# Kernel optimization log

Measured on AMD Instinct MI355X. Metric: run time of the kernel, lower is better.

## Reference

```python
import jax, jax.numpy as jnp
import numpy as np

N_NODES = 50000
N_EDGES = 800000
LEAKY_SLOPE = 0.2


def _gcn_conv(x, src, dst, W, b, n_nodes):
    """DGL GraphConv with norm='both': D_out^{-1/2} -> SpMM -> D_in^{-1/2} -> XW+b.
    Degrees clamped to min 1 as in DGL."""
    ones = jnp.ones(src.shape[0], dtype=x.dtype)
    out_deg = jnp.clip(jax.ops.segment_sum(ones, src, num_segments=n_nodes), 1.0)
    in_deg = jnp.clip(jax.ops.segment_sum(ones, dst, num_segments=n_nodes), 1.0)
    xs = x * jax.lax.rsqrt(out_deg)[:, None]          # [N, F] source-side norm
    agg = jax.ops.segment_sum(xs[src], dst, num_segments=n_nodes)  # SpMM: [N, F]
    agg = agg * jax.lax.rsqrt(in_deg)[:, None]        # dest-side norm
    return agg @ W + b


def setup_inputs() -> dict:
    key = jax.random.key(0)
    ks = jax.random.split(key, 13)
    d_in, d_hid, d_out = 300, 400, 512
    sc_in, sc_hid = 1.0 / np.sqrt(d_in), 1.0 / np.sqrt(d_hid)
    return {
        "init_emb": jax.random.normal(ks[0], (N_NODES, d_in), jnp.float32),
        "Wa1": jax.random.normal(ks[1], (d_in, d_hid), jnp.float32) * sc_in,
        "ba1": jnp.zeros((d_hid,), jnp.float32),
        "Wa2": jax.random.normal(ks[2], (d_hid, d_out), jnp.float32) * sc_hid,
        "ba2": jnp.zeros((d_out,), jnp.float32),
        "Wb1": jax.random.normal(ks[3], (d_in, d_hid), jnp.float32) * sc_in,
        "bb1": jnp.zeros((d_hid,), jnp.float32),
        "Wb2": jax.random.normal(ks[4], (d_hid, d_out), jnp.float32) * sc_hid,
        "bb2": jnp.zeros((d_out,), jnp.float32),
        "src1": jax.random.randint(ks[5], (N_EDGES,), 0, N_NODES, jnp.int32),
        "dst1": jax.random.randint(ks[6], (N_EDGES,), 0, N_NODES, jnp.int32),
        "src2": jax.random.randint(ks[7], (N_EDGES,), 0, N_NODES, jnp.int32),
        "dst2": jax.random.randint(ks[8], (N_EDGES,), 0, N_NODES, jnp.int32),
    }


def reference(init_emb, Wa1, ba1, Wa2, ba2, Wb1, bb1, Wb2, bb2,
              src1, dst1, src2, dst2):
    n = init_emb.shape[0]
    # hop 1 (dropout=0.0 -> identity)
    x1 = jax.nn.leaky_relu(_gcn_conv(init_emb, src1, dst1, Wa1, ba1, n), LEAKY_SLOPE)
    x2 = jax.nn.leaky_relu(_gcn_conv(init_emb, src2, dst2, Wb1, bb1, n), LEAKY_SLOPE)
    x = x1 + x2
    # hop 2
    y1 = _gcn_conv(x, src1, dst1, Wa2, ba2, n)
    y2 = _gcn_conv(x, src2, dst2, Wb2, bb2, n)
    return y1 + y2
```

## Files before the change

### kernel.cpp

```cpp
#include <hip/hip_runtime.h>

#define NN 50000
#define NE 800000
#define LEAKY 0.2f

using bf16x8 = __attribute__((ext_vector_type(8))) short;
using f32x4  = __attribute__((ext_vector_type(4))) float;

static __device__ __forceinline__ unsigned short f2bf(float f) {
  unsigned u = __float_as_uint(f);
  u += 0x7FFF + ((u >> 16) & 1);
  return (unsigned short)(u >> 16);
}
static __device__ __forceinline__ float bf2f(unsigned short h) {
  return __uint_as_float((unsigned)h << 16);
}

__global__ void zero_ints(int* __restrict__ p, int n) {
  int i = blockIdx.x * blockDim.x + threadIdx.x;
  int s = gridDim.x * blockDim.x;
  for (; i < n; i += s) p[i] = 0;
}

__global__ void deg_kernel(const int* __restrict__ s1, const int* __restrict__ d1,
                           const int* __restrict__ s2, const int* __restrict__ d2,
                           int* od1, int* id1, int* od2, int* id2) {
  int i = blockIdx.x * blockDim.x + threadIdx.x;
  int st = gridDim.x * blockDim.x;
  for (int e = i; e < NE; e += st) {
    int a = s1[e], b = d1[e], c = s2[e], d = d2[e];
    atomicAdd(&od1[a], 1);
    atomicAdd(&id1[b], 1);
    atomicAdd(&od2[c], 1);
    atomicAdd(&id2[d], 1);
  }
}

__global__ void scale_kernel(const int* __restrict__ od1, const int* __restrict__ id1,
                             const int* __restrict__ od2, const int* __restrict__ id2,
                             float* io1, float* ii1, float* io2, float* ii2) {
  int i = blockIdx.x * blockDim.x + threadIdx.x;
  if (i < NN) {
    io1[i] = rsqrtf((float)(od1[i] > 0 ? od1[i] : 1));
    ii1[i] = rsqrtf((float)(id1[i] > 0 ? id1[i] : 1));
    io2[i] = rsqrtf((float)(od2[i] > 0 ? od2[i] : 1));
    ii2[i] = rsqrtf((float)(id2[i] > 0 ? id2[i] : 1));
  }
}

__global__ void scan_kernel(const int* __restrict__ id1, const int* __restrict__ id2,
                            int* rp1, int* rp2) {
  const int* deg = blockIdx.x ? id2 : id1;
  int* rp = blockIdx.x ? rp2 : rp1;
  __shared__ int sm[1024];
  __shared__ int carry;
  int t = threadIdx.x;
  if (t == 0) carry = 0;
  __syncthreads();
  for (int base = 0; base < NN; base += 1024) {
    int v = (base + t < NN) ? deg[base + t] : 0;
    sm[t] = v;
    __syncthreads();
    #pragma unroll
    for (int o = 1; o < 1024; o <<= 1) {
      int add = (t >= o) ? sm[t - o] : 0;
      __syncthreads();
      sm[t] += add;
      __syncthreads();
    }
    if (base + t < NN) rp[base + t] = carry + sm[t] - v;
    __syncthreads();
    if (t == 0) carry += sm[1023];
    __syncthreads();
  }
  if (t == 0) rp[NN] = carry;
}

__global__ void fill_kernel(const int* __restrict__ s1, const int* __restrict__ d1,
                            const int* __restrict__ s2, const int* __restrict__ d2,
                            const int* __restrict__ rp1, const int* __restrict__ rp2,
                            int* fill1, int* fill2, int* col1, int* col2) {
  int i = blockIdx.x * blockDim.x + threadIdx.x;
  int st = gridDim.x * blockDim.x;
  for (int e = i; e < NE; e += st) {
    int sa = s1[e], da = d1[e], sb = s2[e], db = d2[e];
    int pa = atomicAdd(&fill1[da], 1);
    int pb = atomicAdd(&fill2[db], 1);
    col1[rp1[da] + pa] = sa;
    col2[rp2[db] + pb] = sb;
  }
}

template <int F>
__global__ __launch_bounds__(256) void spmm_kernel(
    const float* __restrict__ x, const int* __restrict__ rp, const int* __restrict__ col,
    const float* __restrict__ inv_out, const float* __restrict__ inv_in,
    float* __restrict__ outbuf) {
  constexpr int F4 = F / 4;
  constexpr int NI = (F4 + 63) / 64;
  int gw = (blockIdx.x * blockDim.x + threadIdx.x) >> 6;
  int lane = threadIdx.x & 63;
  int nw = (gridDim.x * blockDim.x) >> 6;
  const float4* __restrict__ x4 = (const float4*)x;
  float4* __restrict__ o4 = (float4*)outbuf;
  for (int node = gw; node < NN; node += nw) {
    float4 acc[NI];
    #pragma unroll
    for (int i = 0; i < NI; ++i) acc[i] = make_float4(0.f, 0.f, 0.f, 0.f);
    int beg = rp[node], end = rp[node + 1];
    for (int j = beg; j < end; ++j) {
      int s = col[j];
      float w = inv_out[s];
      #pragma unroll
      for (int i = 0; i < NI; ++i) {
        int idx = i * 64 + lane;
        if (idx < F4) {
          float4 v = x4[(size_t)s * F4 + idx];
          acc[i].x += v.x * w;
          acc[i].y += v.y * w;
          acc[i].z += v.z * w;
          acc[i].w += v.w * w;
        }
      }
    }
    float wi = inv_in[node];
    #pragma unroll
    for (int i = 0; i < NI; ++i) {
      int idx = i * 64 + lane;
      if (idx < F4) {
        float4 v = acc[i];
        v.x *= wi; v.y *= wi; v.z *= wi; v.w *= wi;
        o4[(size_t)node * F4 + idx] = v;
      }
    }
  }
}

__global__ void wsplit(const float* __restrict__ W, short* __restrict__ Wh,
                       short* __restrict__ Wl, int K, int Nc, int KB) {
  int total = 4 * KB * 4096;
  int i = blockIdx.x * blockDim.x + threadIdx.x;
  int st = gridDim.x * blockDim.x;
  for (; i < total; i += st) {
    int chunk = i >> 12;
    int e = i & 4095;
    int kk = e >> 7;
    int rn = e & 127;
    int nb = chunk / KB;
    int kb = chunk - nb * KB;
    int n = nb * 128 + rn;
    int k = kb * 32 + kk;
    float v = (n < Nc && k < K) ? W[(size_t)k * Nc + n] : 0.f;
    unsigned short h = f2bf(v);
    unsigned short l = f2bf(v - bf2f(h));
    size_t o = ((size_t)chunk * 128 + rn) * 32 + kk;
    Wh[o] = (short)h;
    Wl[o] = (short)l;
  }
}

template <int EPI, int DUAL>
__global__ __launch_bounds__(256, 2) void mgemm(
    const float* __restrict__ A1, const float* __restrict__ A2,
    const short* __restrict__ W1h, const short* __restrict__ W1l,
    const short* __restrict__ W2h, const short* __restrict__ W2l,
    const float* __restrict__ b1, const float* __restrict__ b2,
    const float* __restrict__ T, float* __restrict__ out,
    int M, int K, int Nc, int KB) {
  __shared__ short Ah[128 * 40];
  __shared__ short Al[128 * 40];
  __shared__ short Bh[128 * 40];
  __shared__ short Bl[128 * 40];

  const int tid = threadIdx.x;
  const int m0 = blockIdx.y * 128;
  const int nb = blockIdx.x;
  const int n0 = nb * 128;

  const int lane = tid & 63;
  const int wid = tid >> 6;
  const int wr = (wid >> 1) * 64;
  const int wc = (wid & 1) * 64;
  const int lr = lane & 15;
  const int lk = (lane >> 4) * 8;

  f32x4 acc[4][4];
  #pragma unroll
  for (int i = 0; i < 4; ++i)
    #pragma unroll
    for (int j = 0; j < 4; ++j) acc[i][j] = (f32x4)(0.f);

  const int sr = tid >> 1;
  const int sk = (tid & 1) * 16;

  for (int kb = 0; kb < KB; ++kb) {
    {
      const float* arow = A1 + (size_t)(m0 + sr) * K + kb * 32 + sk;
      bool rok = (m0 + sr) < M;
      #pragma unroll
      for (int i4 = 0; i4 < 4; ++i4) {
        int kg = kb * 32 + sk + i4 * 4;
        float4 v = make_float4(0.f, 0.f, 0.f, 0.f);
        if (rok && kg + 4 <= K) v = *(const float4*)(arow + i4 * 4);
        unsigned short hx = f2bf(v.x), hy = f2bf(v.y), hz = f2bf(v.z), hw = f2bf(v.w);
        short4 h = make_short4((short)hx, (short)hy, (short)hz, (short)hw);
        short4 l = make_short4((short)f2bf(v.x - bf2f(hx)), (short)f2bf(v.y - bf2f(hy)),
                               (short)f2bf(v.z - bf2f(hz)), (short)f2bf(v.w - bf2f(hw)));
        *(short4*)&Ah[sr * 40 + sk + i4 * 4] = h;
        *(short4*)&Al[sr * 40 + sk + i4 * 4] = l;
      }
      size_t wbase = (((size_t)nb * KB + kb) << 12) + sr * 32 + sk;
      const uint4* sh = (const uint4*)(W1h + wbase);
      const uint4* sl = (const uint4*)(W1l + wbase);
      *(uint4*)&Bh[sr * 40 + sk]     = sh[0];
      *(uint4*)&Bh[sr * 40 + sk + 8] = sh[1];
      *(uint4*)&Bl[sr * 40 + sk]     = sl[0];
      *(uint4*)&Bl[sr * 40 + sk + 8] = sl[1];
    }
    __syncthreads();
    {
      bf16x8 fah[4], fal[4], fbh[4], fbl[4];
      #pragma unroll
      for (int i = 0; i < 4; ++i) {
        fah[i] = *(const bf16x8*)&Ah[(wr + i * 16 + lr) * 40 + lk];
        fal[i] = *(const bf16x8*)&Al[(wr + i * 16 + lr) * 40 + lk];
      }
      #pragma unroll
      for (int j = 0; j < 4; ++j) {
        fbh[j] = *(const bf16x8*)&Bh[(wc + j * 16 + lr) * 40 + lk];
        fbl[j] = *(const bf16x8*)&Bl[(wc + j * 16 + lr) * 40 + lk];
      }
      #pragma unroll
      for (int i = 0; i < 4; ++i)
        #pragma unroll
        for (int j = 0; j < 4; ++j) {
          acc[i][j] = __builtin_amdgcn_mfma_f32_16x16x32_bf16(fah[i], fbh[j], acc[i][j], 0, 0, 0);
          acc[i][j] = __builtin_amdgcn_mfma_f32_16x16x32_bf16(fah[i], fbl[j], acc[i][j], 0, 0, 0);
          acc[i][j] = __builtin_amdgcn_mfma_f32_16x16x32_bf16(fal[i], fbh[j], acc[i][j], 0, 0, 0);
        }
    }
    __syncthreads();
    if (DUAL) {
      {
        const float* arow = A2 + (size_t)(m0 + sr) * K + kb * 32 + sk;
        bool rok = (m0 + sr) < M;
        #pragma unroll
        for (int i4 = 0; i4 < 4; ++i4) {
          int kg = kb * 32 + sk + i4 * 4;
          float4 v = make_float4(0.f, 0.f, 0.f, 0.f);
          if (rok && kg + 4 <= K) v = *(const float4*)(arow + i4 * 4);
          unsigned short hx = f2bf(v.x), hy = f2bf(v.y), hz = f2bf(v.z), hw = f2bf(v.w);
          short4 h = make_short4((short)hx, (short)hy, (short)hz, (short)hw);
          short4 l = make_short4((short)f2bf(v.x - bf2f(hx)), (short)f2bf(v.y - bf2f(hy)),
                                 (short)f2bf(v.z - bf2f(hz)), (short)f2bf(v.w - bf2f(hw)));
          *(short4*)&Ah[sr * 40 + sk + i4 * 4] = h;
          *(short4*)&Al[sr * 40 + sk + i4 * 4] = l;
        }
        size_t wbase = (((size_t)nb * KB + kb) << 12) + sr * 32 + sk;
        const uint4* sh = (const uint4*)(W2h + wbase);
        const uint4* sl = (const uint4*)(W2l + wbase);
        *(uint4*)&Bh[sr * 40 + sk]     = sh[0];
        *(uint4*)&Bh[sr * 40 + sk + 8] = sh[1];
        *(uint4*)&Bl[sr * 40 + sk]     = sl[0];
        *(uint4*)&Bl[sr * 40 + sk + 8] = sl[1];
      }
      __syncthreads();
      {
        bf16x8 fah[4], fal[4], fbh[4], fbl[4];
        #pragma unroll
        for (int i = 0; i < 4; ++i) {
          fah[i] = *(const bf16x8*)&Ah[(wr + i * 16 + lr) * 40 + lk];
          fal[i] = *(const bf16x8*)&Al[(wr + i * 16 + lr) * 40 + lk];
        }
        #pragma unroll
        for (int j = 0; j < 4; ++j) {
          fbh[j] = *(const bf16x8*)&Bh[(wc + j * 16 + lr) * 40 + lk];
          fbl[j] = *(const bf16x8*)&Bl[(wc + j * 16 + lr) * 40 + lk];
        }
        #pragma unroll
        for (int i = 0; i < 4; ++i)
          #pragma unroll
          for (int j = 0; j < 4; ++j) {
            acc[i][j] = __builtin_amdgcn_mfma_f32_16x16x32_bf16(fah[i], fbh[j], acc[i][j], 0, 0, 0);
            acc[i][j] = __builtin_amdgcn_mfma_f32_16x16x32_bf16(fah[i], fbl[j], acc[i][j], 0, 0, 0);
            acc[i][j] = __builtin_amdgcn_mfma_f32_16x16x32_bf16(fal[i], fbh[j], acc[i][j], 0, 0, 0);
          }
      }
      __syncthreads();
    }
  }

  #pragma unroll
  for (int i = 0; i < 4; ++i) {
    #pragma unroll
    for (int rr = 0; rr < 4; ++rr) {
      int r = m0 + wr + i * 16 + (lane >> 4) * 4 + rr;
      if (r >= M) continue;
      #pragma unroll
      for (int j = 0; j < 4; ++j) {
        int c = n0 + wc + j * 16 + lr;
        if (c >= Nc) continue;
        float v = acc[i][j][rr] + b1[c];
        if (DUAL) v += b2[c];
        if (EPI == 0 || EPI == 1) v = v > 0.f ? v : LEAKY * v;
        if (EPI == 1) v += T[(size_t)r * Nc + c];
        out[(size_t)r * Nc + c] = v;
      }
    }
  }
}

extern "C" void kernel_launch(void* const* d_in, const int* in_sizes, int n_in,
                              void* d_out, int out_size, void* d_ws, size_t ws_size,
                              hipStream_t stream) {
  const float* emb = (const float*)d_in[0];
  const float* Wa1 = (const float*)d_in[1];
  const float* ba1 = (const float*)d_in[2];
  const float* Wa2 = (const float*)d_in[3];
  const float* ba2 = (const float*)d_in[4];
  const float* Wb1 = (const float*)d_in[5];
  const float* bb1 = (const float*)d_in[6];
  const float* Wb2 = (const float*)d_in[7];
  const float* bb2 = (const float*)d_in[8];
  const int* src1 = (const int*)d_in[9];
  const int* dst1 = (const int*)d_in[10];
  const int* src2 = (const int*)d_in[11];
  const int* dst2 = (const int*)d_in[12];
  float* out = (float*)d_out;

  char* ws = (char*)d_ws;
  size_t off = 0;
  auto alloc = [&](size_t nbytes) -> void* {
    off = (off + 255) & ~(size_t)255;
    void* p = ws + off;
    off += nbytes;
    return p;
  };
  int* od1 = (int*)alloc(NN * 4);
  int* id1 = (int*)alloc(NN * 4);
  int* od2 = (int*)alloc(NN * 4);
  int* id2 = (int*)alloc(NN * 4);
  int* fill1 = (int*)alloc(NN * 4);
  int* fill2 = (int*)alloc(NN * 4);
  int* rp1 = (int*)alloc((NN + 1) * 4);
  int* rp2 = (int*)alloc((NN + 1) * 4);
  int* col1 = (int*)alloc((size_t)NE * 4);
  int* col2 = (int*)alloc((size_t)NE * 4);
  float* io1 = (float*)alloc(NN * 4);
  float* ii1 = (float*)alloc(NN * 4);
  float* io2 = (float*)alloc(NN * 4);
  float* ii2 = (float*)alloc(NN * 4);
  const int KB1 = 10;
  const int KB2 = 13;
  short* Wa1h = (short*)alloc((size_t)4 * KB1 * 4096 * 2);
  short* Wa1l = (short*)alloc((size_t)4 * KB1 * 4096 * 2);
  short* Wb1h = (short*)alloc((size_t)4 * KB1 * 4096 * 2);
  short* Wb1l = (short*)alloc((size_t)4 * KB1 * 4096 * 2);
  short* Wa2h = (short*)alloc((size_t)4 * KB2 * 4096 * 2);
  short* Wa2l = (short*)alloc((size_t)4 * KB2 * 4096 * 2);
  short* Wb2h = (short*)alloc((size_t)4 * KB2 * 4096 * 2);
  short* Wb2l = (short*)alloc((size_t)4 * KB2 * 4096 * 2);
  float* bufA1 = (float*)alloc((size_t)NN * 400 * 4);
  float* bufA2 = (float*)alloc((size_t)NN * 400 * 4);
  float* X = (float*)d_out;

  int nz = (int)(((char*)fill2 - (char*)od1) / 4) + NN;
  zero_ints<<<256, 256, 0, stream>>>(od1, nz);

  deg_kernel<<<1024, 256, 0, stream>>>(src1, dst1, src2, dst2, od1, id1, od2, id2);
  scale_kernel<<<(NN + 255) / 256, 256, 0, stream>>>(od1, id1, od2, id2, io1, ii1, io2, ii2);
  scan_kernel<<<2, 1024, 0, stream>>>(id1, id2, rp1, rp2);
  fill_kernel<<<1024, 256, 0, stream>>>(src1, dst1, src2, dst2, rp1, rp2,
                                        fill1, fill2, col1, col2);

  wsplit<<<640, 256, 0, stream>>>(Wa1, Wa1h, Wa1l, 300, 400, KB1);
  wsplit<<<640, 256, 0, stream>>>(Wb1, Wb1h, Wb1l, 300, 400, KB1);
  wsplit<<<832, 256, 0, stream>>>(Wa2, Wa2h, Wa2l, 400, 512, KB2);
  wsplit<<<832, 256, 0, stream>>>(Wb2, Wb2h, Wb2l, 400, 512, KB2);

  dim3 gg(4, (NN + 127) / 128);

  spmm_kernel<300><<<12500, 256, 0, stream>>>(emb, rp1, col1, io1, ii1, bufA1);
  mgemm<0, 0><<<gg, 256, 0, stream>>>(bufA1, nullptr, Wa1h, Wa1l, nullptr, nullptr,
                                      ba1, nullptr, nullptr, X, NN, 300, 400, KB1);
  spmm_kernel<300><<<12500, 256, 0, stream>>>(emb, rp2, col2, io2, ii2, bufA2);
  mgemm<1, 0><<<gg, 256, 0, stream>>>(bufA2, nullptr, Wb1h, Wb1l, nullptr, nullptr,
                                      bb1, nullptr, X, X, NN, 300, 400, KB1);

  spmm_kernel<400><<<12500, 256, 0, stream>>>(X, rp1, col1, io1, ii1, bufA1);
  spmm_kernel<400><<<12500, 256, 0, stream>>>(X, rp2, col2, io2, ii2, bufA2);
  mgemm<2, 1><<<gg, 256, 0, stream>>>(bufA1, bufA2, Wa2h, Wa2l, Wb2h, Wb2l,
                                      ba2, bb2, nullptr, out, NN, 400, 512, KB2);
}
```

Baseline: 1.734 ms.

## Emit bf16 hi/lo split from SpMM and widen GEMM tiles to 128x256

The SpMM epilogue now writes padded bf16 hi/lo pairs directly, so the GEMM no longer reads fp32 activations and converts them per tile. Weights are pre-arranged in an MFMA-fragment-friendly layout, and the GEMM uses 128x256 tiles with 8 accumulator columns per wave and an XCD-aware workgroup remap. The main intent is fewer global bytes read per GEMM and less conversion work. The cost is more registers and less occupancy (the launch-bounds min-blocks hint is removed) plus extra bytes written by the SpMM.

```diff
diff --git a/kernel.cpp b/kernel.cpp
--- a/kernel.cpp
+++ b/kernel.cpp
@@ -91,18 +91,18 @@
   }
 }
 
-template <int F>
+template <int F, int KP>
 __global__ __launch_bounds__(256) void spmm_kernel(
     const float* __restrict__ x, const int* __restrict__ rp, const int* __restrict__ col,
     const float* __restrict__ inv_out, const float* __restrict__ inv_in,
-    float* __restrict__ outbuf) {
+    short* __restrict__ hi, short* __restrict__ lo) {
   constexpr int F4 = F / 4;
-  constexpr int NI = (F4 + 63) / 64;
+  constexpr int P4 = KP / 4;
+  constexpr int NI = (P4 + 63) / 64;
   int gw = (blockIdx.x * blockDim.x + threadIdx.x) >> 6;
   int lane = threadIdx.x & 63;
   int nw = (gridDim.x * blockDim.x) >> 6;
   const float4* __restrict__ x4 = (const float4*)x;
-  float4* __restrict__ o4 = (float4*)outbuf;
   for (int node = gw; node < NN; node += nw) {
     float4 acc[NI];
     #pragma unroll
@@ -127,10 +127,15 @@
     #pragma unroll
     for (int i = 0; i < NI; ++i) {
       int idx = i * 64 + lane;
-      if (idx < F4) {
+      if (idx < P4) {
         float4 v = acc[i];
         v.x *= wi; v.y *= wi; v.z *= wi; v.w *= wi;
-        o4[(size_t)node * F4 + idx] = v;
+        unsigned short hx = f2bf(v.x), hy = f2bf(v.y), hz = f2bf(v.z), hw = f2bf(v.w);
+        short4 h = make_short4((short)hx, (short)hy, (short)hz, (short)hw);
+        short4 l = make_short4((short)f2bf(v.x - bf2f(hx)), (short)f2bf(v.y - bf2f(hy)),
+                               (short)f2bf(v.z - bf2f(hz)), (short)f2bf(v.w - bf2f(hw)));
+        *(short4*)&hi[(size_t)node * KP + idx * 4] = h;
+        *(short4*)&lo[(size_t)node * KP + idx * 4] = l;
       }
     }
   }
@@ -138,153 +143,111 @@
 
 __global__ void wsplit(const float* __restrict__ W, short* __restrict__ Wh,
                        short* __restrict__ Wl, int K, int Nc, int KB) {
-  int total = 4 * KB * 4096;
+  int total = 2 * KB * 8192;
   int i = blockIdx.x * blockDim.x + threadIdx.x;
   int st = gridDim.x * blockDim.x;
   for (; i < total; i += st) {
-    int chunk = i >> 12;
-    int e = i & 4095;
-    int kk = e >> 7;
-    int rn = e & 127;
-    int nb = chunk / KB;
-    int kb = chunk - nb * KB;
-    int n = nb * 128 + rn;
+    int c2 = i >> 13;
+    int e = i & 8191;
+    int kk = e >> 8;
+    int rn = e & 255;
+    int nb2 = c2 / KB;
+    int kb = c2 - nb2 * KB;
+    int n = nb2 * 256 + rn;
     int k = kb * 32 + kk;
     float v = (n < Nc && k < K) ? W[(size_t)k * Nc + n] : 0.f;
     unsigned short h = f2bf(v);
     unsigned short l = f2bf(v - bf2f(h));
-    size_t o = ((size_t)chunk * 128 + rn) * 32 + kk;
+    size_t o = (size_t)c2 * 8192 + (rn >> 4) * 512 + ((kk >> 3) * 16 + (rn & 15)) * 8 + (kk & 7);
     Wh[o] = (short)h;
     Wl[o] = (short)l;
   }
 }
 
 template <int EPI, int DUAL>
-__global__ __launch_bounds__(256, 2) void mgemm(
-    const float* __restrict__ A1, const float* __restrict__ A2,
+__global__ __launch_bounds__(256) void mgemm(
+    const short* __restrict__ A1h, const short* __restrict__ A1l,
+    const short* __restrict__ A2h, const short* __restrict__ A2l,
     const short* __restrict__ W1h, const short* __restrict__ W1l,
     const short* __restrict__ W2h, const short* __restrict__ W2l,
     const float* __restrict__ b1, const float* __restrict__ b2,
     const float* __restrict__ T, float* __restrict__ out,
-    int M, int K, int Nc, int KB) {
-  __shared__ short Ah[128 * 40];
-  __shared__ short Al[128 * 40];
-  __shared__ short Bh[128 * 40];
-  __shared__ short Bl[128 * 40];
+    int M, int Nc, int KB, int KP) {
+  __shared__ short Ah[4096], Al[4096];
+  __shared__ short Bh[8192], Bl[8192];
 
   const int tid = threadIdx.x;
-  const int m0 = blockIdx.y * 128;
-  const int nb = blockIdx.x;
-  const int n0 = nb * 128;
+  const int nwg = gridDim.x;
+  const int q = nwg >> 3, r = nwg & 7;
+  const int xcd = blockIdx.x & 7, loc = blockIdx.x >> 3;
+  const int wgid = ((xcd < r) ? xcd * (q + 1) : r * (q + 1) + (xcd - r) * q) + loc;
+  const int nb = wgid & 1;
+  const int m0 = (wgid >> 1) * 128;
+  const int n0 = nb * 256;
 
   const int lane = tid & 63;
   const int wid = tid >> 6;
   const int wr = (wid >> 1) * 64;
-  const int wc = (wid & 1) * 64;
-  const int lr = lane & 15;
-  const int lk = (lane >> 4) * 8;
-
-  f32x4 acc[4][4];
+  const int wc = (wid & 1) * 128;
+
+  f32x4 acc[4][8];
   #pragma unroll
   for (int i = 0; i < 4; ++i)
     #pragma unroll
-    for (int j = 0; j < 4; ++j) acc[i][j] = (f32x4)(0.f);
-
-  const int sr = tid >> 1;
-  const int sk = (tid & 1) * 16;
+    for (int j = 0; j < 8; ++j) acc[i][j] = (f32x4)(0.f);
 
   for (int kb = 0; kb < KB; ++kb) {
-    {
-      const float* arow = A1 + (size_t)(m0 + sr) * K + kb * 32 + sk;
-      bool rok = (m0 + sr) < M;
+    #pragma unroll
+    for (int ch = 0; ch < 1 + DUAL; ++ch) {
+      const short* __restrict__ Asrch = ch ? A2h : A1h;
+      const short* __restrict__ Asrcl = ch ? A2l : A1l;
+      const short* __restrict__ Wsrch = ch ? W2h : W1h;
+      const short* __restrict__ Wsrcl = ch ? W2l : W1l;
       #pragma unroll
-      for (int i4 = 0; i4 < 4; ++i4) {
-        int kg = kb * 32 + sk + i4 * 4;
-        float4 v = make_float4(0.f, 0.f, 0.f, 0.f);
-        if (rok && kg + 4 <= K) v = *(const float4*)(arow + i4 * 4);
-        unsigned short hx = f2bf(v.x), hy = f2bf(v.y), hz = f2bf(v.z), hw = f2bf(v.w);
-        short4 h = make_short4((short)hx, (short)hy, (short)hz, (short)hw);
-        short4 l = make_short4((short)f2bf(v.x - bf2f(hx)), (short)f2bf(v.y - bf2f(hy)),
-                               (short)f2bf(v.z - bf2f(hz)), (short)f2bf(v.w - bf2f(hw)));
-        *(short4*)&Ah[sr * 40 + sk + i4 * 4] = h;
-        *(short4*)&Al[sr * 40 + sk + i4 * 4] = l;
-      }
-      size_t wbase = (((size_t)nb * KB + kb) << 12) + sr * 32 + sk;
-      const uint4* sh = (const uint4*)(W1h + wbase);
-      const uint4* sl = (const uint4*)(W1l + wbase);
-      *(uint4*)&Bh[sr * 40 + sk]     = sh[0];
-      *(uint4*)&Bh[sr * 40 + sk + 8] = sh[1];
-      *(uint4*)&Bl[sr * 40 + sk]     = sl[0];
-      *(uint4*)&Bl[sr * 40 + sk + 8] = sl[1];
-    }
-    __syncthreads();
-    {
-      bf16x8 fah[4], fal[4], fbh[4], fbl[4];
-      #pragma unroll
-      for (int i = 0; i < 4; ++i) {
-        fah[i] = *(const bf16x8*)&Ah[(wr + i * 16 + lr) * 40 + lk];
-        fal[i] = *(const bf16x8*)&Al[(wr + i * 16 + lr) * 40 + lk];
-      }
-      #pragma unroll
-      for (int j = 0; j < 4; ++j) {
-        fbh[j] = *(const bf16x8*)&Bh[(wc + j * 16 + lr) * 40 + lk];
-        fbl[j] = *(const bf16x8*)&Bl[(wc + j * 16 + lr) * 40 + lk];
-      }
-      #pragma unroll
-      for (int i = 0; i < 4; ++i)
+      for (int it = 0; it < 2; ++it) {
+        int g = it * 256 + tid;
+        int w = g & 63;
+        int rrow = m0 + (g >> 6) * 16 + (w & 15);
+        int ko = (w >> 4) * 8;
+        uint4 vh = make_uint4(0u, 0u, 0u, 0u), vl = vh;
+        if (rrow < M) {
+          size_t ga = (size_t)rrow * KP + kb * 32 + ko;
+          vh = *(const uint4*)(Asrch + ga);
+          vl = *(const uint4*)(Asrcl + ga);
+        }
+        *(uint4*)&Ah[g * 8] = vh;
+        *(uint4*)&Al[g * 8] = vl;
+      }
+      {
+        size_t wb = ((size_t)(nb * KB + kb)) * 8192;
         #pragma unroll
-        for (int j = 0; j < 4; ++j) {
-          acc[i][j] = __builtin_amdgcn_mfma_f32_16x16x32_bf16(fah[i], fbh[j], acc[i][j], 0, 0, 0);
-          acc[i][j] = __builtin_amdgcn_mfma_f32_16x16x32_bf16(fah[i], fbl[j], acc[i][j], 0, 0, 0);
-          acc[i][j] = __builtin_amdgcn_mfma_f32_16x16x32_bf16(fal[i], fbh[j], acc[i][j], 0, 0, 0);
-        }
-    }
-    __syncthreads();
-    if (DUAL) {
-      {
-        const float* arow = A2 + (size_t)(m0 + sr) * K + kb * 32 + sk;
-        bool rok = (m0 + sr) < M;
-        #pragma unroll
-        for (int i4 = 0; i4 < 4; ++i4) {
-          int kg = kb * 32 + sk + i4 * 4;
-          float4 v = make_float4(0.f, 0.f, 0.f, 0.f);
-          if (rok && kg + 4 <= K) v = *(const float4*)(arow + i4 * 4);
-          unsigned short hx = f2bf(v.x), hy = f2bf(v.y), hz = f2bf(v.z), hw = f2bf(v.w);
-          short4 h = make_short4((short)hx, (short)hy, (short)hz, (short)hw);
-          short4 l = make_short4((short)f2bf(v.x - bf2f(hx)), (short)f2bf(v.y - bf2f(hy)),
-                                 (short)f2bf(v.z - bf2f(hz)), (short)f2bf(v.w - bf2f(hw)));
-          *(short4*)&Ah[sr * 40 + sk + i4 * 4] = h;
-          *(short4*)&Al[sr * 40 + sk + i4 * 4] = l;
-        }
-        size_t wbase = (((size_t)nb * KB + kb) << 12) + sr * 32 + sk;
-        const uint4* sh = (const uint4*)(W2h + wbase);
-        const uint4* sl = (const uint4*)(W2l + wbase);
-        *(uint4*)&Bh[sr * 40 + sk]     = sh[0];
-        *(uint4*)&Bh[sr * 40 + sk + 8] = sh[1];
-        *(uint4*)&Bl[sr * 40 + sk]     = sl[0];
-        *(uint4*)&Bl[sr * 40 + sk + 8] = sl[1];
+        for (int it = 0; it < 4; ++it) {
+          int g = it * 256 + tid;
+          *(uint4*)&Bh[g * 8] = *(const uint4*)(Wsrch + wb + g * 8);
+          *(uint4*)&Bl[g * 8] = *(const uint4*)(Wsrcl + wb + g * 8);
+        }
       }
       __syncthreads();
       {
-        bf16x8 fah[4], fal[4], fbh[4], fbl[4];
+        bf16x8 fah[4], fal[4];
         #pragma unroll
         for (int i = 0; i < 4; ++i) {
-          fah[i] = *(const bf16x8*)&Ah[(wr + i * 16 + lr) * 40 + lk];
-          fal[i] = *(const bf16x8*)&Al[(wr + i * 16 + lr) * 40 + lk];
+          int sub = (wr >> 4) + i;
+          fah[i] = *(const bf16x8*)&Ah[sub * 512 + lane * 8];
+          fal[i] = *(const bf16x8*)&Al[sub * 512 + lane * 8];
         }
         #pragma unroll
-        for (int j = 0; j < 4; ++j) {
-          fbh[j] = *(const bf16x8*)&Bh[(wc + j * 16 + lr) * 40 + lk];
-          fbl[j] = *(const bf16x8*)&Bl[(wc + j * 16 + lr) * 40 + lk];
-        }
-        #pragma unroll
-        for (int i = 0; i < 4; ++i)
+        for (int j = 0; j < 8; ++j) {
+          int sub = (wc >> 4) + j;
+          bf16x8 fbh = *(const bf16x8*)&Bh[sub * 512 + lane * 8];
+          bf16x8 fbl = *(const bf16x8*)&Bl[sub * 512 + lane * 8];
           #pragma unroll
-          for (int j = 0; j < 4; ++j) {
-            acc[i][j] = __builtin_amdgcn_mfma_f32_16x16x32_bf16(fah[i], fbh[j], acc[i][j], 0, 0, 0);
-            acc[i][j] = __builtin_amdgcn_mfma_f32_16x16x32_bf16(fah[i], fbl[j], acc[i][j], 0, 0, 0);
-            acc[i][j] = __builtin_amdgcn_mfma_f32_16x16x32_bf16(fal[i], fbh[j], acc[i][j], 0, 0, 0);
+          for (int i = 0; i < 4; ++i) {
+            acc[i][j] = __builtin_amdgcn_mfma_f32_16x16x32_bf16(fah[i], fbh, acc[i][j], 0, 0, 0);
+            acc[i][j] = __builtin_amdgcn_mfma_f32_16x16x32_bf16(fah[i], fbl, acc[i][j], 0, 0, 0);
+            acc[i][j] = __builtin_amdgcn_mfma_f32_16x16x32_bf16(fal[i], fbh, acc[i][j], 0, 0, 0);
           }
+        }
       }
       __syncthreads();
     }
@@ -294,17 +257,17 @@
   for (int i = 0; i < 4; ++i) {
     #pragma unroll
     for (int rr = 0; rr < 4; ++rr) {
-      int r = m0 + wr + i * 16 + (lane >> 4) * 4 + rr;
-      if (r >= M) continue;
+      int rg = m0 + wr + i * 16 + (lane >> 4) * 4 + rr;
+      if (rg >= M) continue;
       #pragma unroll
-      for (int j = 0; j < 4; ++j) {
-        int c = n0 + wc + j * 16 + lr;
+      for (int j = 0; j < 8; ++j) {
+        int c = n0 + wc + j * 16 + (lane & 15);
         if (c >= Nc) continue;
         float v = acc[i][j][rr] + b1[c];
         if (DUAL) v += b2[c];
         if (EPI == 0 || EPI == 1) v = v > 0.f ? v : LEAKY * v;
-        if (EPI == 1) v += T[(size_t)r * Nc + c];
-        out[(size_t)r * Nc + c] = v;
+        if (EPI == 1) v += T[(size_t)rg * Nc + c];
+        out[(size_t)rg * Nc + c] = v;
       }
     }
   }
@@ -352,16 +315,18 @@
   float* ii2 = (float*)alloc(NN * 4);
   const int KB1 = 10;
   const int KB2 = 13;
-  short* Wa1h = (short*)alloc((size_t)4 * KB1 * 4096 * 2);
-  short* Wa1l = (short*)alloc((size_t)4 * KB1 * 4096 * 2);
-  short* Wb1h = (short*)alloc((size_t)4 * KB1 * 4096 * 2);
-  short* Wb1l = (short*)alloc((size_t)4 * KB1 * 4096 * 2);
-  short* Wa2h = (short*)alloc((size_t)4 * KB2 * 4096 * 2);
-  short* Wa2l = (short*)alloc((size_t)4 * KB2 * 4096 * 2);
-  short* Wb2h = (short*)alloc((size_t)4 * KB2 * 4096 * 2);
-  short* Wb2l = (short*)alloc((size_t)4 * KB2 * 4096 * 2);
-  float* bufA1 = (float*)alloc((size_t)NN * 400 * 4);
-  float* bufA2 = (float*)alloc((size_t)NN * 400 * 4);
+  short* Wa1h = (short*)alloc((size_t)2 * KB1 * 8192 * 2);
+  short* Wa1l = (short*)alloc((size_t)2 * KB1 * 8192 * 2);
+  short* Wb1h = (short*)alloc((size_t)2 * KB1 * 8192 * 2);
+  short* Wb1l = (short*)alloc((size_t)2 * KB1 * 8192 * 2);
+  short* Wa2h = (short*)alloc((size_t)2 * KB2 * 8192 * 2);
+  short* Wa2l = (short*)alloc((size_t)2 * KB2 * 8192 * 2);
+  short* Wb2h = (short*)alloc((size_t)2 * KB2 * 8192 * 2);
+  short* Wb2l = (short*)alloc((size_t)2 * KB2 * 8192 * 2);
+  short* A1h = (short*)alloc((size_t)NN * 416 * 2);
+  short* A1l = (short*)alloc((size_t)NN * 416 * 2);
+  short* A2h = (short*)alloc((size_t)NN * 416 * 2);
+  short* A2l = (short*)alloc((size_t)NN * 416 * 2);
   float* X = (float*)d_out;
 
   int nz = (int)(((char*)fill2 - (char*)od1) / 4) + NN;
@@ -373,22 +338,24 @@
   fill_kernel<<<1024, 256, 0, stream>>>(src1, dst1, src2, dst2, rp1, rp2,
                                         fill1, fill2, col1, col2);
 
-  wsplit<<<640, 256, 0, stream>>>(Wa1, Wa1h, Wa1l, 300, 400, KB1);
-  wsplit<<<640, 256, 0, stream>>>(Wb1, Wb1h, Wb1l, 300, 400, KB1);
-  wsplit<<<832, 256, 0, stream>>>(Wa2, Wa2h, Wa2l, 400, 512, KB2);
-  wsplit<<<832, 256, 0, stream>>>(Wb2, Wb2h, Wb2l, 400, 512, KB2);
-
-  dim3 gg(4, (NN + 127) / 128);
-
-  spmm_kernel<300><<<12500, 256, 0, stream>>>(emb, rp1, col1, io1, ii1, bufA1);
-  mgemm<0, 0><<<gg, 256, 0, stream>>>(bufA1, nullptr, Wa1h, Wa1l, nullptr, nullptr,
-                                      ba1, nullptr, nullptr, X, NN, 300, 400, KB1);
-  spmm_kernel<300><<<12500, 256, 0, stream>>>(emb, rp2, col2, io2, ii2, bufA2);
-  mgemm<1, 0><<<gg, 256, 0, stream>>>(bufA2, nullptr, Wb1h, Wb1l, nullptr, nullptr,
-                                      bb1, nullptr, X, X, NN, 300, 400, KB1);
-
-  spmm_kernel<400><<<12500, 256, 0, stream>>>(X, rp1, col1, io1, ii1, bufA1);
-  spmm_kernel<400><<<12500, 256, 0, stream>>>(X, rp2, col2, io2, ii2, bufA2);
-  mgemm<2, 1><<<gg, 256, 0, stream>>>(bufA1, bufA2, Wa2h, Wa2l, Wb2h, Wb2l,
-                                      ba2, bb2, nullptr, out, NN, 400, 512, KB2);
-}
+  wsplit<<<320, 256, 0, stream>>>(Wa1, Wa1h, Wa1l, 300, 400, KB1);
+  wsplit<<<320, 256, 0, stream>>>(Wb1, Wb1h, Wb1l, 300, 400, KB1);
+  wsplit<<<416, 256, 0, stream>>>(Wa2, Wa2h, Wa2l, 400, 512, KB2);
+  wsplit<<<416, 256, 0, stream>>>(Wb2, Wb2h, Wb2l, 400, 512, KB2);
+
+  const int NWG = 2 * ((NN + 127) / 128);
+
+  spmm_kernel<300, 320><<<12500, 256, 0, stream>>>(emb, rp1, col1, io1, ii1, A1h, A1l);
+  mgemm<0, 0><<<NWG, 256, 0, stream>>>(A1h, A1l, nullptr, nullptr, Wa1h, Wa1l,
+                                       nullptr, nullptr, ba1, nullptr, nullptr, X,
+                                       NN, 400, KB1, 320);
+  spmm_kernel<300, 320><<<12500, 256, 0, stream>>>(emb, rp2, col2, io2, ii2, A1h, A1l);
+  mgemm<1, 0><<<NWG, 256, 0, stream>>>(A1h, A1l, nullptr, nullptr, Wb1h, Wb1l,
+                                       nullptr, nullptr, bb1, nullptr, X, X,
+                                       NN, 400, KB1, 320);
+
+  spmm_kernel<400, 416><<<12500, 256, 0, stream>>>(X, rp1, col1, io1, ii1, A1h, A1l);
+  spmm_kernel<400, 416><<<12500, 256, 0, stream>>>(X, rp2, col2, io2, ii2, A2h, A2l);
+  mgemm<2, 1><<<NWG, 256, 0, stream>>>(A1h, A1l, A2h, A2l, Wa2h, Wa2l, Wb2h, Wb2l,
+                                       ba2, bb2, nullptr, out, NN, 512, KB2, 416);
+}
```

Result: slower. 1.872 ms (+8.0%).
